# Performance work log

Measured on AMD Instinct MI355X. Metric: run time of the kernel, lower is better.

Reference implementation:

```python
import jax, jax.numpy as jnp
import numpy as np

IN_DIM = 64
OUT_DIM = 64
NUM_SPLINES = 8
DEGREE = 3
EPS = 1e-8


def setup_inputs() -> dict:
    key = jax.random.key(0)
    k1, k2 = jax.random.split(key, 2)
    x = jax.random.normal(k1, (4, 512, IN_DIM), dtype=jnp.float32)
    control_points = jax.random.normal(k2, (OUT_DIM, IN_DIM, NUM_SPLINES), dtype=jnp.float32) * 0.1
    K = NUM_SPLINES + DEGREE + 1  # 12 knots
    knots = jnp.broadcast_to(jnp.linspace(-1.0, 1.0, K, dtype=jnp.float32), (OUT_DIM, IN_DIM, K)).copy()
    activation_weights = jnp.ones((OUT_DIM, IN_DIM, 4), dtype=jnp.float32) / 4.0
    return {"x": x, "control_points": control_points, "knots": knots, "activation_weights": activation_weights}


def _bspline_basis(x, knots, degree):
    # x: (b, n, d); knots: (O, d, K) -> basis (b, O, n, d, K-degree-1)
    xs = x[:, None, :, :, None]          # (b, 1, n, d, 1)
    t = knots[None, :, None, :, :]       # (1, O, 1, d, K)
    # Cox-de Boor degree 0: indicator of half-open knot interval
    B = ((xs >= t[..., :-1]) & (xs < t[..., 1:])).astype(x.dtype)  # (b, O, n, d, K-1)
    for k in range(1, degree + 1):
        Km = B.shape[-1]
        c1 = (xs - t[..., : Km - 1]) / (t[..., k : k + Km - 1] - t[..., : Km - 1] + EPS)
        c2 = (t[..., k + 1 : k + Km] - xs) / (t[..., k + 1 : k + Km] - t[..., 1:Km] + EPS)
        B = c1 * B[..., :-1] + c2 * B[..., 1:]
    return B


def reference(x, control_points, knots, activation_weights):
    # B-spline branch: (b,O,n,d,S) x (O,d,S) -> (b,O,n)
    basis = _bspline_basis(x, knots, DEGREE)
    out = jnp.einsum('bonds,ods->bon', basis, control_points)
    # activation-mixture branch: activations are independent of the out dim
    acts = jnp.stack([jax.nn.relu(x), jnp.tanh(x), jax.nn.sigmoid(x), x], axis=-1)  # (b,n,d,4)
    act_out = jnp.einsum('bnda,oda->bon', acts, activation_weights)
    return out + 0.1 * act_out  # (b, out_dim, n)
```

## Files before the change

kernel.cpp:

```cpp
#include <hip/hip_runtime.h>

#define D_IN 64
#define D_OUT 64
#define NS 8
#define NK 12
#define NREC 13
#define KAN_EPS 1e-8f

__device__ float4 g_rec[D_OUT * D_IN * NREC];
__device__ float4 g_m1[D_OUT * D_IN];
__device__ float2 g_m2[D_OUT * D_IN];

struct P4 { float c0, c1, c2, c3; };
__device__ inline P4 p_scal(P4 p, float s) { return {p.c0*s, p.c1*s, p.c2*s, p.c3*s}; }
__device__ inline P4 p_add(P4 a, P4 b) { return {a.c0+b.c0, a.c1+b.c1, a.c2+b.c2, a.c3+b.c3}; }
__device__ inline P4 p_mul_xma(P4 p, float a) { return {-a*p.c0, p.c0 - a*p.c1, p.c1 - a*p.c2, p.c2 - a*p.c3}; }
__device__ inline P4 p_mul_bmx(P4 p, float b) { return {b*p.c0, b*p.c1 - p.c0, b*p.c2 - p.c1, b*p.c3 - p.c2}; }

__global__ __launch_bounds__(256)
void kan_prep_all(const float* __restrict__ cp,
                  const float* __restrict__ knots,
                  const float* __restrict__ aw,
                  const float* __restrict__ x,
                  float4* __restrict__ acts)
{
    const int blk = blockIdx.x;
    const int tid = threadIdx.x;

    if (blk < 208) {
        int flat = blk * 256 + tid;
        int iv13 = flat % NREC;
        int od   = flat / NREC;

        float t[NK];
        #pragma unroll
        for (int j = 0; j < NK; ++j) t[j] = knots[od * NK + j];
        auto tk = [&](int j) -> float {
            if (j < 0)  return t[0]  + (float)j;
            if (j > 11) return t[11] + (float)(j - 11);
            return t[j];
        };

        P4 sp = {0.f, 0.f, 0.f, 0.f};
        int iv = iv13 - 1;
        if (iv >= 0 && iv <= 10) {
            float tL0 = tk(iv),   tL1 = tk(iv-1), tL2 = tk(iv-2);
            float tR1 = tk(iv+1), tR2 = tk(iv+2), tR3 = tk(iv+3);
            float R1  = 1.f / (tR1 - tL0 + KAN_EPS);
            float R2a = 1.f / (tR1 - tL1 + KAN_EPS);
            float R2b = 1.f / (tR2 - tL0 + KAN_EPS);
            float R3a = 1.f / (tR1 - tL2 + KAN_EPS);
            float R3b = 1.f / (tR2 - tL1 + KAN_EPS);
            float R3c = 1.f / (tR3 - tL0 + KAN_EPS);

            P4 N0 = {1.f, 0.f, 0.f, 0.f}, N1, N2, N3, t0p, t1p, t2p, sv;
            t0p = p_scal(N0, R1);
            N0 = p_mul_bmx(t0p, tR1);
            N1 = p_mul_xma(t0p, tL0);
            t0p = p_scal(N0, R2a);
            N0 = p_mul_bmx(t0p, tR1);
            sv = p_mul_xma(t0p, tL1);
            t1p = p_scal(N1, R2b);
            N1 = p_add(sv, p_mul_bmx(t1p, tR2));
            N2 = p_mul_xma(t1p, tL0);
            t0p = p_scal(N0, R3a);
            N0 = p_mul_bmx(t0p, tR1);
            sv = p_mul_xma(t0p, tL2);
            t1p = p_scal(N1, R3b);
            N1 = p_add(sv, p_mul_bmx(t1p, tR2));
            sv = p_mul_xma(t1p, tL1);
            t2p = p_scal(N2, R3c);
            N2 = p_add(sv, p_mul_bmx(t2p, tR3));
            N3 = p_mul_xma(t2p, tL0);

            float cpv[4];
            #pragma unroll
            for (int r = 0; r < 4; ++r) {
                int i = iv - 3 + r;
                cpv[r] = (i >= 0 && i <= 7) ? cp[od * NS + i] : 0.f;
            }
            sp = p_add(p_add(p_scal(N0, cpv[0]), p_scal(N1, cpv[1])),
                       p_add(p_scal(N2, cpv[2]), p_scal(N3, cpv[3])));
        }
        float w1 = aw[od * 4 + 1];
        float w3 = aw[od * 4 + 3];
        sp.c0 -= 0.1f * w1;
        sp.c1 += 0.1f * w3;
        g_rec[flat] = make_float4(sp.c0, sp.c1, sp.c2, sp.c3);

    } else if (blk < 224) {
        int od = (blk - 208) * 256 + tid;
        const float* t = knots + od * NK;
        float t0 = t[0];
        float h  = (t[11] - t0) * (1.0f / 11.0f);
        bool uni = (h > 0.0f);
        #pragma unroll
        for (int j = 0; j < 11; ++j)
            uni = uni && (fabsf((t[j + 1] - t[j]) - h) <= fmaxf(1e-6f, 1e-4f * fabsf(h)));
        float w0 = aw[od * 4 + 0];
        float w1 = aw[od * 4 + 1];
        float w2 = aw[od * 4 + 2];
        g_m1[od] = make_float4(t0, uni ? 1.0f / h : 0.0f, uni ? 1.0f : 0.0f, w0);
        g_m2[od] = make_float2(2.0f * w1, w2);

    } else {
        int idx = (blk - 224) * 256 + tid;
        int d  = idx >> 11;
        int bn = idx & 2047;
        float xv = x[bn * D_IN + d];
        float v  = __expf(-xv);
        float Ra = __builtin_amdgcn_rcpf(1.f + v * v);
        float Rb = __builtin_amdgcn_rcpf(1.f + v);
        acts[idx] = make_float4(fmaxf(xv, 0.f), Ra, Rb, 0.f);
    }
}

__global__ __launch_bounds__(256)
void kan_main(const float* __restrict__ x,
              const float* __restrict__ knots,
              const float4* __restrict__ acts,
              float* __restrict__ out)
{
    __shared__ float s_red[4][64];

    const int o   = blockIdx.y;
    const int bnl = threadIdx.x & 63;
    const int dq  = threadIdx.x >> 6;
    const int bn  = blockIdx.x * 64 + bnl;
    const int d0  = dq * 16;

    const float4* xp = (const float4*)(x + bn * D_IN + d0);
    float4 xa = xp[0], xb = xp[1], xc = xp[2], xd = xp[3];
    float xs[16] = {xa.x, xa.y, xa.z, xa.w, xb.x, xb.y, xb.z, xb.w,
                    xc.x, xc.y, xc.z, xc.w, xd.x, xd.y, xd.z, xd.w};

    float acc  = 0.f;
    float aacc = 0.f;

    #pragma unroll
    for (int i = 0; i < 16; ++i) {
        const int d  = d0 + i;
        const int od = __builtin_amdgcn_readfirstlane(o * D_IN + d);
        const float xv = xs[i];

        const float4 m1 = g_m1[od];
        int cnt;
        if (__builtin_amdgcn_readfirstlane(__float_as_int(m1.z))) {
            float u  = (xv - m1.x) * m1.y;
            float cf = fminf(fmaxf(floorf(u) + 1.0f, 0.0f), 12.0f);
            cnt = (int)cf;
        } else {
            const float* __restrict__ kt = knots + od * NK;
            cnt = 0;
            #pragma unroll
            for (int j = 0; j < NK; ++j) cnt += (xv >= kt[j]) ? 1 : 0;
        }

        const float4 cf4 = g_rec[od * NREC + cnt];
        acc += ((cf4.w * xv + cf4.z) * xv + cf4.y) * xv + cf4.x;

        const float2 m2 = g_m2[od];
        const float4 a  = acts[(d << 11) + bn];
        aacc += a.x * m1.w + a.y * m2.x + a.z * m2.y;
    }

    s_red[dq][bnl] = acc + 0.1f * aacc;
    __syncthreads();

    if (dq == 0) {
        float r = s_red[0][bnl] + s_red[1][bnl] + s_red[2][bnl] + s_red[3][bnl];
        const int b = bn >> 9;
        const int n = bn & 511;
        out[((b * D_OUT + o) << 9) | n] = r;
    }
}

extern "C" void kernel_launch(void* const* d_in, const int* in_sizes, int n_in,
                              void* d_out, int out_size, void* d_ws, size_t ws_size,
                              hipStream_t stream) {
    const float* x     = (const float*)d_in[0];
    const float* cp    = (const float*)d_in[1];
    const float* knots = (const float*)d_in[2];
    const float* aw    = (const float*)d_in[3];
    float* out = (float*)d_out;
    float4* acts = (float4*)d_ws;

    kan_prep_all<<<736, 256, 0, stream>>>(cp, knots, aw, x, acts);

    dim3 grid(2048 / 64, D_OUT);
    kan_main<<<grid, 256, 0, stream>>>(x, knots, acts, out);
}
```

Before: 26.28 us.

## Precompute per-(bn,d) interval index and powers, detect knot sharing across outputs

The prep kernel now computes each x value's knot interval count once per (bn,d), using the d-th knot row, along with x, x^2 and x^3. It also flags whether the knot rows are identical across all output dims. When they are, the main kernel skips per-output interval search and just gathers coefficients and does FMAs. The main kernel is retiled to 512 threads covering 8 outputs x 32 rows x 2 d-halves, with split accumulators. The trade-off is extra workspace traffic (two float4 arrays) and a slower fallback path that loads knots per element when rows differ.

```diff
diff --git a/kernel.cpp b/kernel.cpp
--- a/kernel.cpp
+++ b/kernel.cpp
@@ -8,8 +8,8 @@
 #define KAN_EPS 1e-8f
 
 __device__ float4 g_rec[D_OUT * D_IN * NREC];
-__device__ float4 g_m1[D_OUT * D_IN];
-__device__ float2 g_m2[D_OUT * D_IN];
+__device__ float4 g_awf[D_OUT * D_IN];
+__device__ int    g_mism[16];
 
 struct P4 { float c0, c1, c2, c3; };
 __device__ inline P4 p_scal(P4 p, float s) { return {p.c0*s, p.c1*s, p.c2*s, p.c3*s}; }
@@ -22,7 +22,8 @@
                   const float* __restrict__ knots,
                   const float* __restrict__ aw,
                   const float* __restrict__ x,
-                  float4* __restrict__ acts)
+                  float4* __restrict__ P1,
+                  float4* __restrict__ P2)
 {
     const int blk = blockIdx.x;
     const int tid = threadIdx.x;
@@ -90,88 +91,111 @@
 
     } else if (blk < 224) {
         int od = (blk - 208) * 256 + tid;
-        const float* t = knots + od * NK;
-        float t0 = t[0];
-        float h  = (t[11] - t0) * (1.0f / 11.0f);
-        bool uni = (h > 0.0f);
-        #pragma unroll
-        for (int j = 0; j < 11; ++j)
-            uni = uni && (fabsf((t[j + 1] - t[j]) - h) <= fmaxf(1e-6f, 1e-4f * fabsf(h)));
         float w0 = aw[od * 4 + 0];
         float w1 = aw[od * 4 + 1];
         float w2 = aw[od * 4 + 2];
-        g_m1[od] = make_float4(t0, uni ? 1.0f / h : 0.0f, uni ? 1.0f : 0.0f, w0);
-        g_m2[od] = make_float2(2.0f * w1, w2);
+        g_awf[od] = make_float4(w0, 2.0f * w1, w2, 0.0f);
+
+        int d = od & 63;
+        int m = 0;
+        #pragma unroll
+        for (int j = 0; j < NK; ++j)
+            m |= (knots[od * NK + j] != knots[d * NK + j]) ? 1 : 0;
+        __shared__ int sm;
+        if (tid == 0) sm = 0;
+        __syncthreads();
+        if (m) atomicOr(&sm, 1);
+        __syncthreads();
+        if (tid == 0) g_mism[blk - 208] = sm;
 
     } else {
         int idx = (blk - 224) * 256 + tid;
-        int d  = idx >> 11;
-        int bn = idx & 2047;
-        float xv = x[bn * D_IN + d];
+        int bn = idx >> 6, d = idx & 63;
+        float xv = x[idx];
+        int cnt = 0;
+        #pragma unroll
+        for (int j = 0; j < NK; ++j) cnt += (xv >= knots[d * NK + j]) ? 1 : 0;
         float v  = __expf(-xv);
         float Ra = __builtin_amdgcn_rcpf(1.f + v * v);
         float Rb = __builtin_amdgcn_rcpf(1.f + v);
-        acts[idx] = make_float4(fmaxf(xv, 0.f), Ra, Rb, 0.f);
+        P1[(d << 11) + bn] = make_float4(xv, xv * xv, xv * xv * xv, (float)cnt);
+        P2[(d << 11) + bn] = make_float4(fmaxf(xv, 0.f), Ra, Rb, 0.f);
     }
 }
 
-__global__ __launch_bounds__(256)
-void kan_main(const float* __restrict__ x,
+__global__ __launch_bounds__(512)
+void kan_main(const float4* __restrict__ P1,
+              const float4* __restrict__ P2,
               const float* __restrict__ knots,
-              const float4* __restrict__ acts,
               float* __restrict__ out)
 {
-    __shared__ float s_red[4][64];
-
-    const int o   = blockIdx.y;
-    const int bnl = threadIdx.x & 63;
-    const int dq  = threadIdx.x >> 6;
-    const int bn  = blockIdx.x * 64 + bnl;
-    const int d0  = dq * 16;
-
-    const float4* xp = (const float4*)(x + bn * D_IN + d0);
-    float4 xa = xp[0], xb = xp[1], xc = xp[2], xd = xp[3];
-    float xs[16] = {xa.x, xa.y, xa.z, xa.w, xb.x, xb.y, xb.z, xb.w,
-                    xc.x, xc.y, xc.z, xc.w, xd.x, xd.y, xd.z, xd.w};
-
-    float acc  = 0.f;
-    float aacc = 0.f;
-
+    __shared__ float s_red[256];
+
+    const int tid = threadIdx.x;
+    const int bnl = tid & 31;
+    const int og  = (tid >> 5) & 7;
+    const int dh  = tid >> 8;
+    const int bn  = blockIdx.x * 32 + bnl;
+    const int o   = blockIdx.y * 8 + og;
+    const int dbase = dh << 5;
+
+    int mm = 0;
     #pragma unroll
-    for (int i = 0; i < 16; ++i) {
-        const int d  = d0 + i;
-        const int od = __builtin_amdgcn_readfirstlane(o * D_IN + d);
-        const float xv = xs[i];
-
-        const float4 m1 = g_m1[od];
-        int cnt;
-        if (__builtin_amdgcn_readfirstlane(__float_as_int(m1.z))) {
-            float u  = (xv - m1.x) * m1.y;
-            float cf = fminf(fmaxf(floorf(u) + 1.0f, 0.0f), 12.0f);
-            cnt = (int)cf;
-        } else {
-            const float* __restrict__ kt = knots + od * NK;
-            cnt = 0;
+    for (int k = 0; k < 16; ++k) mm |= g_mism[k];
+
+    float a0 = 0.f, a1 = 0.f, w0acc = 0.f, w1acc = 0.f;
+
+    if (mm == 0) {
+        #pragma unroll 4
+        for (int i = 0; i < 32; ++i) {
+            const int d  = dbase + i;
+            const int od = (o << 6) + d;
+            const float4 p1 = P1[(d << 11) + bn];
+            const float4 p2 = P2[(d << 11) + bn];
+            const float4 cf = g_rec[od * NREC + (int)p1.w];
+            float t = fmaf(cf.y, p1.x, cf.x);
+            t = fmaf(cf.z, p1.y, t);
+            t = fmaf(cf.w, p1.z, t);
+            const float4 w = g_awf[od];
+            float s = p2.x * w.x;
+            s = fmaf(p2.y, w.y, s);
+            s = fmaf(p2.z, w.z, s);
+            if (i & 1) { a1 += t; w1acc += s; }
+            else       { a0 += t; w0acc += s; }
+        }
+    } else {
+        #pragma unroll 2
+        for (int i = 0; i < 32; ++i) {
+            const int d  = dbase + i;
+            const int od = (o << 6) + d;
+            const float4 p1 = P1[(d << 11) + bn];
+            const float4 p2 = P2[(d << 11) + bn];
+            const float xv = p1.x;
+            int cnt = 0;
             #pragma unroll
-            for (int j = 0; j < NK; ++j) cnt += (xv >= kt[j]) ? 1 : 0;
+            for (int j = 0; j < NK; ++j) cnt += (xv >= knots[od * NK + j]) ? 1 : 0;
+            const float4 cf = g_rec[od * NREC + cnt];
+            float t = fmaf(cf.y, p1.x, cf.x);
+            t = fmaf(cf.z, p1.y, t);
+            t = fmaf(cf.w, p1.z, t);
+            const float4 w = g_awf[od];
+            float s = p2.x * w.x;
+            s = fmaf(p2.y, w.y, s);
+            s = fmaf(p2.z, w.z, s);
+            if (i & 1) { a1 += t; w1acc += s; }
+            else       { a0 += t; w0acc += s; }
         }
-
-        const float4 cf4 = g_rec[od * NREC + cnt];
-        acc += ((cf4.w * xv + cf4.z) * xv + cf4.y) * xv + cf4.x;
-
-        const float2 m2 = g_m2[od];
-        const float4 a  = acts[(d << 11) + bn];
-        aacc += a.x * m1.w + a.y * m2.x + a.z * m2.y;
     }
 
-    s_red[dq][bnl] = acc + 0.1f * aacc;
+    float tot = (a0 + a1) + 0.1f * (w0acc + w1acc);
+
+    if (dh) s_red[tid & 255] = tot;
     __syncthreads();
-
-    if (dq == 0) {
-        float r = s_red[0][bnl] + s_red[1][bnl] + s_red[2][bnl] + s_red[3][bnl];
+    if (!dh) {
+        tot += s_red[tid];
         const int b = bn >> 9;
         const int n = bn & 511;
-        out[((b * D_OUT + o) << 9) | n] = r;
+        out[(((b << 6) + o) << 9) | n] = tot;
     }
 }
 
@@ -183,10 +207,12 @@
     const float* knots = (const float*)d_in[2];
     const float* aw    = (const float*)d_in[3];
     float* out = (float*)d_out;
-    float4* acts = (float4*)d_ws;
-
-    kan_prep_all<<<736, 256, 0, stream>>>(cp, knots, aw, x, acts);
-
-    dim3 grid(2048 / 64, D_OUT);
-    kan_main<<<grid, 256, 0, stream>>>(x, knots, acts, out);
+
+    float4* P1 = (float4*)d_ws;
+    float4* P2 = P1 + D_IN * 2048;
+
+    kan_prep_all<<<736, 256, 0, stream>>>(cp, knots, aw, x, P1, P2);
+
+    dim3 grid(2048 / 32, D_OUT / 8);
+    kan_main<<<grid, 512, 0, stream>>>(P1, P2, knots, out);
 }
```

New measurement: 29.35 us. 1.12x slower.
